# Optimization experiments

Hardware: AMD Instinct MI355X
Metric: run time of the kernel (lower is better)

The kernel has to match this reference:

```python
import jax, jax.numpy as jnp
import numpy as np

MODES = 16

def setup_inputs() -> dict:
    key = jax.random.key(0)
    k1, k2 = jax.random.split(key)
    x = jax.random.normal(k1, (16, 32, 256, 256), dtype=jnp.float32)
    weights = jax.random.normal(k2, (32, 32, MODES, MODES, 2), dtype=jnp.float32) * 0.1
    return {"x": x, "weights": weights}

def reference(x, weights):
    # x: [B, Ci, H, W]; weights: [Ci, Co, m, m, 2]
    B, Ci, H, W = x.shape
    m = weights.shape[2]
    Co = weights.shape[1]
    x_ft = jnp.fft.rfft2(x, axes=(-2, -1))  # [B, Ci, H, W//2+1] complex
    w_c = jax.lax.complex(weights[..., 0], weights[..., 1])  # [Ci, Co, m, m]
    low = jnp.einsum('bixy,ioxy->boxy', x_ft[:, :, :m, :m], w_c)  # [B, Co, m, m]
    out_ft = jnp.zeros((B, Co, H, W // 2 + 1), dtype=x_ft.dtype)
    out_ft = out_ft.at[:, :, :m, :m].set(low)
    return jnp.fft.irfft2(out_ft, s=(H, W), axes=(-2, -1)).astype(x.dtype)
```

## Files before the change

### kernel.cpp

```cpp
#include <hip/hip_runtime.h>

typedef float v4 __attribute__((ext_vector_type(4)));
typedef float f32x4 __attribute__((ext_vector_type(4)));
typedef short bf16x8 __attribute__((ext_vector_type(8)));

#define TWO_PI_256 0.024543692606170259f


__device__ __forceinline__ unsigned short f2bf(float f) {
  const unsigned int u = __float_as_uint(f);
  return (unsigned short)((u + 0x7fffu + ((u >> 16) & 1u)) >> 16);
}
__device__ __forceinline__ float bf2f(unsigned short h) {
  return __uint_as_float(((unsigned int)h) << 16);
}

__global__ __launch_bounds__(256) void k0_trig(unsigned short* __restrict__ Th,
                                               unsigned short* __restrict__ Tl,
                                               unsigned short* __restrict__ Bh,
                                               unsigned short* __restrict__ Bl) {
  const int k = threadIdx.x;
  const int o = blockIdx.x;
  {
    const int kx = o >> 1, p = o & 1;
    float sv, cv;
    sincosf((float)((kx * k) & 255) * TWO_PI_256, &sv, &cv);
    const float val = p ? -sv : cv;
    const unsigned short hi = f2bf(val);
    Th[o * 256 + k] = hi;
    Tl[o * 256 + k] = f2bf(val - bf2f(hi));
  }
  {
    const int idx = o * 256 + k;
    const int nt = idx >> 9;
    const int lane = (idx >> 3) & 63;
    const int j = idx & 7;
    const int q = lane >> 4;
    const int n16 = lane & 15;
    const int kk = q * 8 + j;
    const int w = nt * 16 + n16;
    float val;
    if (kk == 0) {
      val = 1.f / 65536.f;
    } else if (kk == 16) {
      val = 0.f;
    } else {
      const int kx = kk & 15;
      float sv, cv;
      sincosf((float)((kx * w) & 255) * TWO_PI_256, &sv, &cv);
      val = (kk < 16 ? 2.f * cv : -2.f * sv) * (1.f / 65536.f);
    }
    const unsigned short hi = f2bf(val);
    Bh[idx] = hi;
    Bl[idx] = f2bf(val - bf2f(hi));
  }
}

typedef __attribute__((address_space(1))) const unsigned int gas_u32;
typedef __attribute__((address_space(3))) unsigned int las_u32;

__global__ __launch_bounds__(256) void k1_dftw(const float* __restrict__ x,
                                               const unsigned short* __restrict__ Th,
                                               const unsigned short* __restrict__ Tl,
                                               float* __restrict__ F) {
  __shared__ float Xs[128 * 32];
  __shared__ __align__(16) unsigned short Ts[2][32 * 264];
  const int tid = threadIdx.x;
  const int lane = tid & 63;
  const int w = tid >> 6;
  const long rblk = (long)blockIdx.x * 128;
  {
    const int o = tid >> 3, kb = (tid & 7) * 32;
#pragma unroll
    for (int f = 0; f < 2; ++f) {
      const unsigned short* src = (f ? Tl : Th) + o * 256 + kb;
      unsigned short* dst = &Ts[f][o * 264 + kb];
#pragma unroll
      for (int j = 0; j < 32; j += 8)
        *(bf16x8*)(dst + j) = *(const bf16x8*)(src + j);
    }
  }
  const int q = lane >> 4;
  const int n16 = lane & 15;
  f32x4 acc[2][2] = {};
  for (int kc = 0; kc < 256; kc += 32) {
    __syncthreads();
#pragma unroll
    for (int i = 0; i < 4; ++i) {
      const int r0 = w * 32 + i * 8;
      __builtin_amdgcn_global_load_lds(
          (gas_u32*)(x + (rblk + r0 + (lane >> 3)) * 256 + kc + (lane & 7) * 4),
          (las_u32*)((unsigned int*)Xs + r0 * 32), 16, 0, 0);
    }
    __syncthreads();
    bf16x8 bh[2], bl[2];
#pragma unroll
    for (int nt = 0; nt < 2; ++nt) {
      const int o = nt * 16 + n16;
      bh[nt] = *(const bf16x8*)&Ts[0][o * 264 + kc + q * 8];
      bl[nt] = *(const bf16x8*)&Ts[1][o * 264 + kc + q * 8];
    }
#pragma unroll
    for (int mt = 0; mt < 2; ++mt) {
      const int m = w * 32 + mt * 16 + n16;
      const float* ap = &Xs[m * 32 + q * 8];
      const v4 a0 = *(const v4*)ap;
      const v4 a1 = *(const v4*)(ap + 4);
      const float af[8] = {a0[0], a0[1], a0[2], a0[3], a1[0], a1[1], a1[2], a1[3]};
      bf16x8 ah, al;
#pragma unroll
      for (int j = 0; j < 8; ++j) {
        const unsigned short h = f2bf(af[j]);
        ah[j] = (short)h;
        al[j] = (short)f2bf(af[j] - bf2f(h));
      }
#pragma unroll
      for (int nt = 0; nt < 2; ++nt) {
        acc[mt][nt] = __builtin_amdgcn_mfma_f32_16x16x32_bf16(ah, bh[nt], acc[mt][nt], 0, 0, 0);
        acc[mt][nt] = __builtin_amdgcn_mfma_f32_16x16x32_bf16(al, bh[nt], acc[mt][nt], 0, 0, 0);
        acc[mt][nt] = __builtin_amdgcn_mfma_f32_16x16x32_bf16(ah, bl[nt], acc[mt][nt], 0, 0, 0);
      }
    }
  }
#pragma unroll
  for (int mt = 0; mt < 2; ++mt)
#pragma unroll
    for (int nt = 0; nt < 2; ++nt)
#pragma unroll
      for (int r = 0; r < 4; ++r) {
        const long row = rblk + w * 32 + mt * 16 + q * 4 + r;
        F[row * 32 + nt * 16 + n16] = acc[mt][nt][r];
      }
}

__global__ __launch_bounds__(256) void k2_dfth(const float* __restrict__ F,
                                               float* __restrict__ X) {
  __shared__ float Fs[64][36];
  const int tid = threadIdx.x;
  const int bc = blockIdx.x;
  const int kx = tid & 15;
  const int ky = tid >> 4;
  float sn, cs;
  sincosf((float)ky * TWO_PI_256, &sn, &cs);
  float wr = 1.f, wi = 0.f;
  float xr = 0.f, xi = 0.f;
  const float* Fb = F + (long)bc * 8192;
  for (int hc = 0; hc < 256; hc += 64) {
    __syncthreads();
#pragma unroll
    for (int p = 0; p < 2; ++p) {
      const int h = (tid >> 3) + p * 32;
      const int j = (tid & 7) * 4;
      *(v4*)&Fs[h][j] = *(const v4*)&Fb[(hc + h) * 32 + j];
    }
    __syncthreads();
#pragma unroll 8
    for (int hl = 0; hl < 64; ++hl) {
      const float2 f = *(const float2*)&Fs[hl][2 * kx];
      xr += f.x * wr + f.y * wi;
      xi += f.y * wr - f.x * wi;
      const float nwr = wr * cs - wi * sn;
      const float nwi = wr * sn + wi * cs;
      wr = nwr;
      wi = nwi;
    }
  }
  *(float2*)&X[((long)bc * 256 + tid) * 2] = make_float2(xr, xi);
}

__global__ __launch_bounds__(256) void kB_mixinv(const float* __restrict__ X,
                                                 const float* __restrict__ Wt,
                                                 const unsigned short* __restrict__ Bh,
                                                 const unsigned short* __restrict__ Bl,
                                                 float* __restrict__ out) {
  __shared__ float2 tbl[256];
  __shared__ float2 Ys[256];
  __shared__ float Gs[128][36];
  const int tid = threadIdx.x;
  const int lane = tid & 63;
  const int wv = tid >> 6;
  const int co = blockIdx.x >> 1;
  const int h0 = (blockIdx.x & 1) << 7;
  const int b = blockIdx.y;
  const long bc = b * 32 + co;
  {
    float sv, cv;
    sincosf((float)tid * TWO_PI_256, &sv, &cv);
    tbl[tid] = make_float2(cv, sv);
  }
  {
    float yr = 0.f, yi = 0.f;
    const float2* Xb = (const float2*)X + (long)b * 8192 + tid;
    const float2* Wb = (const float2*)Wt + (long)co * 256 + tid;
#pragma unroll 8
    for (int ci = 0; ci < 32; ++ci) {
      const float2 xv = Xb[ci * 256];
      const float2 wv2 = Wb[ci * 8192];
      yr += xv.x * wv2.x - xv.y * wv2.y;
      yi += xv.x * wv2.y + xv.y * wv2.x;
    }
    Ys[tid] = make_float2(yr, yi);
  }
  __syncthreads();
  {
    const int hl = tid >> 1;
    const int p = tid & 1;
    const int h = h0 + hl;
    float gr[8] = {}, gi[8] = {};
#pragma unroll 4
    for (int ky = 0; ky < 16; ++ky) {
      const float2 wt = tbl[(ky * h) & 255];
#pragma unroll
      for (int i = 0; i < 8; ++i) {
        const float2 yv = Ys[ky * 16 + p * 8 + i];
        gr[i] += yv.x * wt.x - yv.y * wt.y;
        gi[i] += yv.x * wt.y + yv.y * wt.x;
      }
    }
#pragma unroll
    for (int i = 0; i < 8; ++i) {
      const int kx = p * 8 + i;
      Gs[hl][kx] = gr[i];
      Gs[hl][16 + kx] = gi[i];
    }
  }
  __syncthreads();
  const int q = lane >> 4;
  const int n16 = lane & 15;
  bf16x8 ah[2], al[2];
#pragma unroll
  for (int mt = 0; mt < 2; ++mt) {
    const float* ap = &Gs[wv * 32 + mt * 16 + n16][q * 8];
    const v4 a0 = *(const v4*)ap;
    const v4 a1 = *(const v4*)(ap + 4);
    const float af[8] = {a0[0], a0[1], a0[2], a0[3], a1[0], a1[1], a1[2], a1[3]};
#pragma unroll
    for (int j = 0; j < 8; ++j) {
      const unsigned short hh = f2bf(af[j]);
      ah[mt][j] = (short)hh;
      al[mt][j] = (short)f2bf(af[j] - bf2f(hh));
    }
  }
  f32x4 acc[2][16] = {};
#pragma unroll
  for (int nt = 0; nt < 16; ++nt) {
    const bf16x8 bhf = *(const bf16x8*)&Bh[(nt * 64 + lane) * 8];
    const bf16x8 blf = *(const bf16x8*)&Bl[(nt * 64 + lane) * 8];
#pragma unroll
    for (int mt = 0; mt < 2; ++mt) {
      acc[mt][nt] = __builtin_amdgcn_mfma_f32_16x16x32_bf16(ah[mt], bhf, acc[mt][nt], 0, 0, 0);
      acc[mt][nt] = __builtin_amdgcn_mfma_f32_16x16x32_bf16(al[mt], bhf, acc[mt][nt], 0, 0, 0);
      acc[mt][nt] = __builtin_amdgcn_mfma_f32_16x16x32_bf16(ah[mt], blf, acc[mt][nt], 0, 0, 0);
    }
  }
  float* __restrict__ ob = out + bc * 65536;
#pragma unroll
  for (int mt = 0; mt < 2; ++mt)
#pragma unroll
    for (int r = 0; r < 4; ++r) {
      const int h = h0 + wv * 32 + mt * 16 + q * 4 + r;
#pragma unroll
      for (int nt = 0; nt < 16; ++nt)
        ob[h * 256 + nt * 16 + n16] = acc[mt][nt][r];
    }
}

extern "C" void kernel_launch(void* const* d_in, const int* in_sizes, int n_in,
                              void* d_out, int out_size, void* d_ws, size_t ws_size,
                              hipStream_t stream) {
  const float* x = (const float*)d_in[0];
  const float* wt = (const float*)d_in[1];
  float* out = (float*)d_out;
  float* F = (float*)d_ws;
  float* X = F + 4194304;
  unsigned short* Th = (unsigned short*)(X + 262144);
  unsigned short* Tl = Th + 8192;
  unsigned short* Bh = Tl + 8192;
  unsigned short* Bl = Bh + 8192;
  k0_trig<<<32, 256, 0, stream>>>(Th, Tl, Bh, Bl);
  k1_dftw<<<1024, 256, 0, stream>>>(x, Th, Tl, F);
  k2_dfth<<<512, 256, 0, stream>>>(F, X);
  kB_mixinv<<<dim3(64, 16), 256, 0, stream>>>(X, wt, Bh, Bl, out);
}
```

Measured before the change: 295.4 us.

## Fuse width and height DFT kernels per image; widen mixinv blocks to full image

Merges the width-DFT and height-DFT kernels into a single kernel. Each block processes one whole (b,ci) image and keeps the intermediate spectrum in shared memory instead of writing it to and reading it back from global memory. The x loads use an XOR swizzle to avoid LDS bank conflicts. The mix/inverse kernel now uses 512-thread blocks covering all 256 rows, splitting the ci reduction across two halves and storing MFMA results per tile to reduce register use. Tradeoffs: fewer blocks in the DFT kernel, larger shared-memory use that may lower occupancy, and the height-DFT phase running serially after the MFMA phase within each block.

```diff
diff --git a/kernel.cpp b/kernel.cpp
--- a/kernel.cpp
+++ b/kernel.cpp
@@ -59,16 +59,16 @@
 typedef __attribute__((address_space(1))) const unsigned int gas_u32;
 typedef __attribute__((address_space(3))) unsigned int las_u32;
 
-__global__ __launch_bounds__(256) void k1_dftw(const float* __restrict__ x,
+__global__ __launch_bounds__(256) void k12_dft(const float* __restrict__ x,
                                                const unsigned short* __restrict__ Th,
                                                const unsigned short* __restrict__ Tl,
-                                               float* __restrict__ F) {
-  __shared__ float Xs[128 * 32];
+                                               float* __restrict__ X) {
+  __shared__ __align__(16) float SXF[256 * 34];
   __shared__ __align__(16) unsigned short Ts[2][32 * 264];
   const int tid = threadIdx.x;
   const int lane = tid & 63;
   const int w = tid >> 6;
-  const long rblk = (long)blockIdx.x * 128;
+  const long bc = blockIdx.x;
   {
     const int o = tid >> 3, kb = (tid & 7) * 32;
 #pragma unroll
@@ -82,15 +82,16 @@
   }
   const int q = lane >> 4;
   const int n16 = lane & 15;
-  f32x4 acc[2][2] = {};
+  const int ucol = (lane & 7) ^ (lane >> 3);
+  f32x4 acc[4][2] = {};
   for (int kc = 0; kc < 256; kc += 32) {
     __syncthreads();
 #pragma unroll
-    for (int i = 0; i < 4; ++i) {
-      const int r0 = w * 32 + i * 8;
+    for (int i = 0; i < 8; ++i) {
+      const int r0 = w * 64 + i * 8;
       __builtin_amdgcn_global_load_lds(
-          (gas_u32*)(x + (rblk + r0 + (lane >> 3)) * 256 + kc + (lane & 7) * 4),
-          (las_u32*)((unsigned int*)Xs + r0 * 32), 16, 0, 0);
+          (gas_u32*)(x + (bc * 256 + r0 + (lane >> 3)) * 256 + kc + ucol * 4),
+          (las_u32*)((unsigned int*)SXF + r0 * 32), 16, 0, 0);
     }
     __syncthreads();
     bf16x8 bh[2], bl[2];
@@ -101,11 +102,11 @@
       bl[nt] = *(const bf16x8*)&Ts[1][o * 264 + kc + q * 8];
     }
 #pragma unroll
-    for (int mt = 0; mt < 2; ++mt) {
-      const int m = w * 32 + mt * 16 + n16;
-      const float* ap = &Xs[m * 32 + q * 8];
-      const v4 a0 = *(const v4*)ap;
-      const v4 a1 = *(const v4*)(ap + 4);
+    for (int mt = 0; mt < 4; ++mt) {
+      const int m = w * 64 + mt * 16 + n16;
+      const int s = n16 & 7;
+      const v4 a0 = *(const v4*)&SXF[m * 32 + ((2 * q) ^ s) * 4];
+      const v4 a1 = *(const v4*)&SXF[m * 32 + ((2 * q + 1) ^ s) * 4];
       const float af[8] = {a0[0], a0[1], a0[2], a0[3], a1[0], a1[1], a1[2], a1[3]};
       bf16x8 ah, al;
 #pragma unroll
@@ -122,41 +123,25 @@
       }
     }
   }
-#pragma unroll
-  for (int mt = 0; mt < 2; ++mt)
+  __syncthreads();
+#pragma unroll
+  for (int mt = 0; mt < 4; ++mt)
 #pragma unroll
     for (int nt = 0; nt < 2; ++nt)
 #pragma unroll
-      for (int r = 0; r < 4; ++r) {
-        const long row = rblk + w * 32 + mt * 16 + q * 4 + r;
-        F[row * 32 + nt * 16 + n16] = acc[mt][nt][r];
-      }
-}
-
-__global__ __launch_bounds__(256) void k2_dfth(const float* __restrict__ F,
-                                               float* __restrict__ X) {
-  __shared__ float Fs[64][36];
-  const int tid = threadIdx.x;
-  const int bc = blockIdx.x;
-  const int kx = tid & 15;
-  const int ky = tid >> 4;
-  float sn, cs;
-  sincosf((float)ky * TWO_PI_256, &sn, &cs);
-  float wr = 1.f, wi = 0.f;
-  float xr = 0.f, xi = 0.f;
-  const float* Fb = F + (long)bc * 8192;
-  for (int hc = 0; hc < 256; hc += 64) {
-    __syncthreads();
-#pragma unroll
-    for (int p = 0; p < 2; ++p) {
-      const int h = (tid >> 3) + p * 32;
-      const int j = (tid & 7) * 4;
-      *(v4*)&Fs[h][j] = *(const v4*)&Fb[(hc + h) * 32 + j];
-    }
-    __syncthreads();
+      for (int r = 0; r < 4; ++r)
+        SXF[(w * 64 + mt * 16 + q * 4 + r) * 34 + nt * 16 + n16] = acc[mt][nt][r];
+  __syncthreads();
+  {
+    const int kx = tid & 15;
+    const int ky = tid >> 4;
+    float sn, cs;
+    sincosf((float)ky * TWO_PI_256, &sn, &cs);
+    float wr = 1.f, wi = 0.f;
+    float xr = 0.f, xi = 0.f;
 #pragma unroll 8
-    for (int hl = 0; hl < 64; ++hl) {
-      const float2 f = *(const float2*)&Fs[hl][2 * kx];
+    for (int h = 0; h < 256; ++h) {
+      const float2 f = *(const float2*)&SXF[h * 34 + 2 * kx];
       xr += f.x * wr + f.y * wi;
       xi += f.y * wr - f.x * wi;
       const float nwr = wr * cs - wi * sn;
@@ -164,55 +149,60 @@
       wr = nwr;
       wi = nwi;
     }
-  }
-  *(float2*)&X[((long)bc * 256 + tid) * 2] = make_float2(xr, xi);
-}
-
-__global__ __launch_bounds__(256) void kB_mixinv(const float* __restrict__ X,
+    *(float2*)&X[(bc * 256 + tid) * 2] = make_float2(xr, xi);
+  }
+}
+
+__global__ __launch_bounds__(512) void kB_mixinv(const float* __restrict__ X,
                                                  const float* __restrict__ Wt,
                                                  const unsigned short* __restrict__ Bh,
                                                  const unsigned short* __restrict__ Bl,
                                                  float* __restrict__ out) {
   __shared__ float2 tbl[256];
-  __shared__ float2 Ys[256];
-  __shared__ float Gs[128][36];
+  __shared__ float2 Yp[2][256];
+  __shared__ float Gs[256][36];
   const int tid = threadIdx.x;
   const int lane = tid & 63;
   const int wv = tid >> 6;
-  const int co = blockIdx.x >> 1;
-  const int h0 = (blockIdx.x & 1) << 7;
+  const int co = blockIdx.x;
   const int b = blockIdx.y;
   const long bc = b * 32 + co;
-  {
+  const int t2 = tid & 255;
+  const int hf = tid >> 8;
+  if (hf == 0) {
     float sv, cv;
-    sincosf((float)tid * TWO_PI_256, &sv, &cv);
-    tbl[tid] = make_float2(cv, sv);
+    sincosf((float)t2 * TWO_PI_256, &sv, &cv);
+    tbl[t2] = make_float2(cv, sv);
   }
   {
     float yr = 0.f, yi = 0.f;
-    const float2* Xb = (const float2*)X + (long)b * 8192 + tid;
-    const float2* Wb = (const float2*)Wt + (long)co * 256 + tid;
+    const float2* Xp = (const float2*)X + ((long)b * 8192 + t2);
+    const float2* Wp = (const float2*)Wt + ((long)co * 256 + t2);
 #pragma unroll 8
-    for (int ci = 0; ci < 32; ++ci) {
-      const float2 xv = Xb[ci * 256];
-      const float2 wv2 = Wb[ci * 8192];
+    for (int ci = hf * 16; ci < hf * 16 + 16; ++ci) {
+      const float2 xv = Xp[ci * 256];
+      const float2 wv2 = Wp[ci * 8192];
       yr += xv.x * wv2.x - xv.y * wv2.y;
       yi += xv.x * wv2.y + xv.y * wv2.x;
     }
-    Ys[tid] = make_float2(yr, yi);
-  }
-  __syncthreads();
-  {
-    const int hl = tid >> 1;
+    Yp[hf][t2] = make_float2(yr, yi);
+  }
+  __syncthreads();
+  if (tid < 256) {
+    const float2 a = Yp[0][tid], c = Yp[1][tid];
+    Yp[0][tid] = make_float2(a.x + c.x, a.y + c.y);
+  }
+  __syncthreads();
+  {
+    const int h = tid >> 1;
     const int p = tid & 1;
-    const int h = h0 + hl;
     float gr[8] = {}, gi[8] = {};
 #pragma unroll 4
     for (int ky = 0; ky < 16; ++ky) {
       const float2 wt = tbl[(ky * h) & 255];
 #pragma unroll
       for (int i = 0; i < 8; ++i) {
-        const float2 yv = Ys[ky * 16 + p * 8 + i];
+        const float2 yv = Yp[0][ky * 16 + p * 8 + i];
         gr[i] += yv.x * wt.x - yv.y * wt.y;
         gi[i] += yv.x * wt.y + yv.y * wt.x;
       }
@@ -220,8 +210,8 @@
 #pragma unroll
     for (int i = 0; i < 8; ++i) {
       const int kx = p * 8 + i;
-      Gs[hl][kx] = gr[i];
-      Gs[hl][16 + kx] = gi[i];
+      Gs[h][kx] = gr[i];
+      Gs[h][16 + kx] = gi[i];
     }
   }
   __syncthreads();
@@ -241,28 +231,24 @@
       al[mt][j] = (short)f2bf(af[j] - bf2f(hh));
     }
   }
-  f32x4 acc[2][16] = {};
+  float* __restrict__ ob = out + bc * 65536;
 #pragma unroll
   for (int nt = 0; nt < 16; ++nt) {
     const bf16x8 bhf = *(const bf16x8*)&Bh[(nt * 64 + lane) * 8];
     const bf16x8 blf = *(const bf16x8*)&Bl[(nt * 64 + lane) * 8];
-#pragma unroll
-    for (int mt = 0; mt < 2; ++mt) {
-      acc[mt][nt] = __builtin_amdgcn_mfma_f32_16x16x32_bf16(ah[mt], bhf, acc[mt][nt], 0, 0, 0);
-      acc[mt][nt] = __builtin_amdgcn_mfma_f32_16x16x32_bf16(al[mt], bhf, acc[mt][nt], 0, 0, 0);
-      acc[mt][nt] = __builtin_amdgcn_mfma_f32_16x16x32_bf16(ah[mt], blf, acc[mt][nt], 0, 0, 0);
-    }
-  }
-  float* __restrict__ ob = out + bc * 65536;
-#pragma unroll
-  for (int mt = 0; mt < 2; ++mt)
+    f32x4 c0 = {}, c1 = {};
+    c0 = __builtin_amdgcn_mfma_f32_16x16x32_bf16(ah[0], bhf, c0, 0, 0, 0);
+    c0 = __builtin_amdgcn_mfma_f32_16x16x32_bf16(al[0], bhf, c0, 0, 0, 0);
+    c0 = __builtin_amdgcn_mfma_f32_16x16x32_bf16(ah[0], blf, c0, 0, 0, 0);
+    c1 = __builtin_amdgcn_mfma_f32_16x16x32_bf16(ah[1], bhf, c1, 0, 0, 0);
+    c1 = __builtin_amdgcn_mfma_f32_16x16x32_bf16(al[1], bhf, c1, 0, 0, 0);
+    c1 = __builtin_amdgcn_mfma_f32_16x16x32_bf16(ah[1], blf, c1, 0, 0, 0);
 #pragma unroll
     for (int r = 0; r < 4; ++r) {
-      const int h = h0 + wv * 32 + mt * 16 + q * 4 + r;
-#pragma unroll
-      for (int nt = 0; nt < 16; ++nt)
-        ob[h * 256 + nt * 16 + n16] = acc[mt][nt][r];
-    }
+      ob[(wv * 32 + q * 4 + r) * 256 + nt * 16 + n16] = c0[r];
+      ob[(wv * 32 + 16 + q * 4 + r) * 256 + nt * 16 + n16] = c1[r];
+    }
+  }
 }
 
 extern "C" void kernel_launch(void* const* d_in, const int* in_sizes, int n_in,
@@ -271,14 +257,12 @@
   const float* x = (const float*)d_in[0];
   const float* wt = (const float*)d_in[1];
   float* out = (float*)d_out;
-  float* F = (float*)d_ws;
-  float* X = F + 4194304;
+  float* X = (float*)d_ws;
   unsigned short* Th = (unsigned short*)(X + 262144);
   unsigned short* Tl = Th + 8192;
   unsigned short* Bh = Tl + 8192;
   unsigned short* Bl = Bh + 8192;
   k0_trig<<<32, 256, 0, stream>>>(Th, Tl, Bh, Bl);
-  k1_dftw<<<1024, 256, 0, stream>>>(x, Th, Tl, F);
-  k2_dfth<<<512, 256, 0, stream>>>(F, X);
-  kB_mixinv<<<dim3(64, 16), 256, 0, stream>>>(X, wt, Bh, Bl, out);
-}
+  k12_dft<<<512, 256, 0, stream>>>(x, Th, Tl, X);
+  kB_mixinv<<<dim3(32, 16), 512, 0, stream>>>(X, wt, Bh, Bl, out);
+}
```

After: 265.9 us. -10.0%, faster.
